# Kernel optimization log

Hardware: AMD Instinct MI355X
Metric: run time of the kernel (lower is better)

The kernel has to match this reference:

```python
import jax, jax.numpy as jnp
import numpy as np
from jax import lax

EPS = 1e-5

def _conv1d(x, w, b):
    # x: [B,C,L], w: [O,I,K], valid padding, stride 1
    y = lax.conv_general_dilated(x, w, window_strides=(1,), padding='VALID',
                                 dimension_numbers=('NCH', 'OIH', 'NCH'))
    return y + b[None, :, None]

def setup_inputs() -> dict:
    key = jax.random.key(0)
    ks = jax.random.split(key, 7)
    B, L, C = 16, 4096, 512
    x = jax.random.normal(ks[0], (B, L, C), dtype=jnp.float32)
    fan3 = 1.0 / np.sqrt(C * 3)
    fan1 = 1.0 / np.sqrt(C * 1)
    w_down = jax.random.uniform(ks[1], (C, C, 3), jnp.float32, -fan3, fan3)
    b_down = jax.random.uniform(ks[2], (C,), jnp.float32, -fan3, fan3)
    w_pad = jax.random.uniform(ks[3], (C, C, 1), jnp.float32, -fan1, fan1)
    b_pad = jax.random.uniform(ks[4], (C,), jnp.float32, -fan1, fan1)
    gamma = jnp.ones((C,), jnp.float32)
    beta = jnp.zeros((C,), jnp.float32)
    return {"x": x, "w_down": w_down, "b_down": b_down,
            "w_pad": w_pad, "b_pad": b_pad, "gamma": gamma, "beta": beta}

def reference(x, w_down, b_down, w_pad, b_pad, gamma, beta):
    # d == 2 branch of ConvLayer
    B, L, C = x.shape

    def branch(xs):  # xs: [B, L//2, C]
        xt = jnp.transpose(xs, (0, 2, 1))                 # [B,C,L/2]
        p1 = _conv1d(xt, w_down, b_down)                  # [B,C,L/2-2]
        p2 = _conv1d(xt[:, :, :2], w_pad, b_pad)          # [B,C,2]
        return jnp.concatenate([p1, p2], axis=2)          # [B,C,L/2]

    x1_p = branch(x[:, 0::2, :])
    x2_p = branch(x[:, 1::2, :])
    # interleave: even positions from x1_p, odd from x2_p
    x_p = jnp.stack([x1_p, x2_p], axis=3).reshape(B, C, L)

    # BatchNorm1d in training mode: batch stats over (batch, length)
    mean = jnp.mean(x_p, axis=(0, 2), keepdims=True)
    var = jnp.var(x_p, axis=(0, 2), keepdims=True)
    xn = (x_p - mean) * lax.rsqrt(var + EPS)
    xn = xn * gamma[None, :, None] + beta[None, :, None]

    y = jax.nn.elu(xn)                                    # dropout = identity (eval)
    y = y + jnp.transpose(x, (0, 2, 1))                   # residual [B,C,L]

    # MaxPool1d(kernel=3, stride=2, padding=1)
    yp = jnp.pad(y, ((0, 0), (0, 0), (1, 1)), constant_values=-jnp.inf)
    pooled = lax.reduce_window(yp, -jnp.inf, lax.max, (1, 1, 3), (1, 1, 2), 'VALID')
    return jnp.transpose(pooled, (0, 2, 1))               # [B, L//2, C]
```

## Files before the change

kernel.cpp:

```cpp
#include <hip/hip_runtime.h>
#include <hip/hip_bf16.h>
#include <math.h>

typedef __bf16 bf16;
typedef __bf16 bf16x8 __attribute__((ext_vector_type(8)));
typedef float floatx4 __attribute__((ext_vector_type(4)));

#define GAS __attribute__((address_space(1)))
#define LAS __attribute__((address_space(3)))

static constexpr int B_ = 16, L_ = 4096, C_ = 512;
static constexpr int M_ = B_ * L_;
static constexpr int K_ = 3 * C_;

__global__ void cast_x(const float* __restrict__ x, bf16* __restrict__ xb) {
    const size_t i = ((size_t)blockIdx.x * 256 + threadIdx.x) * 8;
    floatx4 a = *(const floatx4*)(x + i);
    floatx4 b = *(const floatx4*)(x + i + 4);
    bf16x8 o;
#pragma unroll
    for (int j = 0; j < 4; ++j) { o[j] = (bf16)a[j]; o[4 + j] = (bf16)b[j]; }
    *(bf16x8*)(xb + i) = o;
}

__global__ void repack_w(const float* __restrict__ wd, bf16* __restrict__ wr) {
    int idx = blockIdx.x * 256 + threadIdx.x;
    int o   = idx / K_;
    int rem = idx - o * K_;
    int kk  = rem >> 9;
    int i   = rem & 511;
    wr[idx] = (bf16)wd[o * K_ + i * 3 + kk];
}

__global__ __launch_bounds__(256) void gemm_conv(
    const bf16* __restrict__ x, const bf16* __restrict__ wr,
    const float* __restrict__ bd, bf16* __restrict__ xp)
{
    __shared__ bf16 As[128 * 32];
    __shared__ bf16 Bs[128 * 32];

    const int tid = threadIdx.x;
    const int nb = blockIdx.x & 3;
    const int mb = blockIdx.x >> 2;
    const int m0 = mb * 128;
    const int n0 = nb * 128;

    const int wave = tid >> 6;
    const int lane = tid & 63;
    const int wm = wave & 1;
    const int wn = wave >> 1;
    const int tm = lane & 15;
    const int quad = lane >> 4;

    floatx4 acc[4][4];
#pragma unroll
    for (int i = 0; i < 4; ++i)
#pragma unroll
        for (int j = 0; j < 4; ++j) acc[i][j] = floatx4{0.f, 0.f, 0.f, 0.f};

    const int qa0 = tid, qa1 = tid + 256;
    const int rowA0 = qa0 >> 2, rowA1 = qa1 >> 2;
    const int seg = (tid & 3) << 3;

    for (int kt = 0; kt < 48; ++kt) {
        const int kk = kt >> 4;
        const int i0 = (kt & 15) << 5;
        {
            int sr0 = m0 + rowA0 + 2 * kk; if (sr0 > M_ - 1) sr0 = M_ - 1;
            int sr1 = m0 + rowA1 + 2 * kk; if (sr1 > M_ - 1) sr1 = M_ - 1;
            const bf16* s0 = x + (size_t)sr0 * C_ + i0 + seg;
            const bf16* s1 = x + (size_t)sr1 * C_ + i0 + seg;
            __builtin_amdgcn_global_load_lds((const GAS void*)s0, (LAS void*)(As + qa0 * 8), 16, 0, 0);
            __builtin_amdgcn_global_load_lds((const GAS void*)s1, (LAS void*)(As + qa1 * 8), 16, 0, 0);
        }
        {
            const bf16* s0 = wr + (size_t)(n0 + rowA0) * K_ + kk * C_ + i0 + seg;
            const bf16* s1 = wr + (size_t)(n0 + rowA1) * K_ + kk * C_ + i0 + seg;
            __builtin_amdgcn_global_load_lds((const GAS void*)s0, (LAS void*)(Bs + qa0 * 8), 16, 0, 0);
            __builtin_amdgcn_global_load_lds((const GAS void*)s1, (LAS void*)(Bs + qa1 * 8), 16, 0, 0);
        }
        __syncthreads();

        bf16x8 af[4], bfr[4];
#pragma unroll
        for (int mi = 0; mi < 4; ++mi)
            af[mi] = *(const bf16x8*)(As + (wm * 64 + mi * 16 + tm) * 32 + quad * 8);
#pragma unroll
        for (int ni = 0; ni < 4; ++ni)
            bfr[ni] = *(const bf16x8*)(Bs + (wn * 64 + ni * 16 + tm) * 32 + quad * 8);
#pragma unroll
        for (int mi = 0; mi < 4; ++mi)
#pragma unroll
            for (int ni = 0; ni < 4; ++ni)
                acc[mi][ni] = __builtin_amdgcn_mfma_f32_16x16x32_bf16(af[mi], bfr[ni], acc[mi][ni], 0, 0, 0);
        __syncthreads();
    }

    float bias[4];
#pragma unroll
    for (int ni = 0; ni < 4; ++ni) bias[ni] = bd[n0 + wn * 64 + ni * 16 + tm];

#pragma unroll
    for (int mi = 0; mi < 4; ++mi) {
#pragma unroll
        for (int r = 0; r < 4; ++r) {
            const int m = m0 + wm * 64 + mi * 16 + quad * 4 + r;
            bf16* dst = xp + (size_t)m * C_ + n0 + wn * 64 + tm;
#pragma unroll
            for (int ni = 0; ni < 4; ++ni)
                dst[ni * 16] = (bf16)(acc[mi][ni][r] + bias[ni]);
        }
    }
}

__global__ void fixup(const float* __restrict__ x, const float* __restrict__ wp,
                      const float* __restrict__ bp, bf16* __restrict__ xp)
{
    const int b = blockIdx.x >> 2;
    const int j = blockIdx.x & 3;
    __shared__ float xrow[C_];
    for (int i = threadIdx.x; i < C_; i += 256)
        xrow[i] = x[(size_t)(b * L_ + j) * C_ + i];
    __syncthreads();
    for (int c = threadIdx.x; c < C_; c += 256) {
        const float* w = wp + (size_t)c * C_;
        float acc = 0.f;
#pragma unroll 4
        for (int i = 0; i < C_; i += 4) {
            floatx4 wv = *(const floatx4*)(w + i);
#pragma unroll
            for (int u = 0; u < 4; ++u) acc += wv[u] * xrow[i + u];
        }
        xp[(size_t)(b * L_ + 4092 + j) * C_ + c] = (bf16)(acc + bp[c]);
    }
}

__global__ void stats_reduce(const bf16* __restrict__ xp, float* __restrict__ sums) {
    const int c = threadIdx.x * 2;
    const size_t r0 = (size_t)blockIdx.x * 256;
    float s0 = 0.f, s1 = 0.f, q0 = 0.f, q1 = 0.f;
    for (int r = 0; r < 256; ++r) {
        const bf16* p = xp + (r0 + r) * C_ + c;
        float v0 = (float)p[0], v1 = (float)p[1];
        s0 += v0; q0 += v0 * v0;
        s1 += v1; q1 += v1 * v1;
    }
    atomicAdd(&sums[c], s0);
    atomicAdd(&sums[c + 1], s1);
    atomicAdd(&sums[C_ + c], q0);
    atomicAdd(&sums[C_ + c + 1], q1);
}

__global__ void finalize_stats(const float* __restrict__ sums, const float* __restrict__ gamma,
                               const float* __restrict__ beta, float* __restrict__ ss) {
    const int c = threadIdx.x;
    const float invn = 1.0f / 65536.0f;
    float mean = sums[c] * invn;
    float var  = sums[C_ + c] * invn - mean * mean;
    float scale = gamma[c] * rsqrtf(var + 1e-5f);
    ss[c] = scale;
    ss[C_ + c] = beta[c] - mean * scale;
}

__global__ void final_pool(const bf16* __restrict__ xp, const float* __restrict__ x,
                           const float* __restrict__ ss, float* __restrict__ out)
{
    const int gid = blockIdx.x * 256 + threadIdx.x;
    const int cg = gid & 63;
    const int t  = (gid >> 6) & 2047;
    const int b  = gid >> 17;
    const int c0 = cg << 3;

    float sc[8], sh[8];
#pragma unroll
    for (int j = 0; j < 8; ++j) { sc[j] = ss[c0 + j]; sh[j] = ss[C_ + c0 + j]; }

    float best[8];
#pragma unroll
    for (int j = 0; j < 8; ++j) best[j] = -INFINITY;

#pragma unroll
    for (int dl = -1; dl <= 1; ++dl) {
        const int l = 2 * t + dl;
        if (l < 0) continue;
        const size_t off = (size_t)(b * L_ + l) * C_ + c0;
        bf16x8 xpv = *(const bf16x8*)(xp + off);
        floatx4 xv0 = *(const floatx4*)(x + off);
        floatx4 xv1 = *(const floatx4*)(x + off + 4);
#pragma unroll
        for (int j = 0; j < 8; ++j) {
            float z = sc[j] * (float)xpv[j] + sh[j];
            float y = (z > 0.f) ? z : (expf(z) - 1.f);
            y += (j < 4) ? xv0[j] : xv1[j - 4];
            best[j] = fmaxf(best[j], y);
        }
    }
    floatx4 o0, o1;
#pragma unroll
    for (int j = 0; j < 4; ++j) { o0[j] = best[j]; o1[j] = best[4 + j]; }
    *(floatx4*)(out + (size_t)gid * 8) = o0;
    *(floatx4*)(out + (size_t)gid * 8 + 4) = o1;
}

extern "C" void kernel_launch(void* const* d_in, const int* in_sizes, int n_in,
                              void* d_out, int out_size, void* d_ws, size_t ws_size,
                              hipStream_t stream)
{
    const float* x      = (const float*)d_in[0];
    const float* w_down = (const float*)d_in[1];
    const float* b_down = (const float*)d_in[2];
    const float* w_pad  = (const float*)d_in[3];
    const float* b_pad  = (const float*)d_in[4];
    const float* gamma  = (const float*)d_in[5];
    const float* beta   = (const float*)d_in[6];
    float* out = (float*)d_out;

    char* ws = (char*)d_ws;
    bf16*  xb   = (bf16*)ws;
    bf16*  xp   = (bf16*)(ws + (size_t)M_ * C_ * 2);
    bf16*  wr   = (bf16*)(ws + (size_t)M_ * C_ * 4);
    float* sums = (float*)(ws + (size_t)M_ * C_ * 4 + (size_t)C_ * K_ * 2);
    float* ss   = sums + 2 * C_;

    hipMemsetAsync(sums, 0, 2 * C_ * sizeof(float), stream);
    cast_x<<<dim3(M_ * C_ / (256 * 8)), dim3(256), 0, stream>>>(x, xb);
    repack_w<<<dim3(3072), dim3(256), 0, stream>>>(w_down, wr);
    gemm_conv<<<dim3(2048), dim3(256), 0, stream>>>(xb, wr, b_down, xp);
    fixup<<<dim3(64), dim3(256), 0, stream>>>(x, w_pad, b_pad, xp);
    stats_reduce<<<dim3(256), dim3(256), 0, stream>>>(xp, sums);
    finalize_stats<<<dim3(1), dim3(512), 0, stream>>>(sums, gamma, beta, ss);
    final_pool<<<dim3(8192), dim3(256), 0, stream>>>(xp, x, ss, out);
}
```

Measured before the change: 468.9 us.

## Fuse BN stats into GEMM epilogue, widen K tile with swizzle, reorder blocks

```diff
diff --git a/kernel.cpp b/kernel.cpp
--- a/kernel.cpp
+++ b/kernel.cpp
@@ -34,16 +34,17 @@
 
 __global__ __launch_bounds__(256) void gemm_conv(
     const bf16* __restrict__ x, const bf16* __restrict__ wr,
-    const float* __restrict__ bd, bf16* __restrict__ xp)
-{
-    __shared__ bf16 As[128 * 32];
-    __shared__ bf16 Bs[128 * 32];
+    const float* __restrict__ bd, bf16* __restrict__ xp, float* __restrict__ sums)
+{
+    __shared__ bf16 As[128 * 64];
+    __shared__ bf16 Bs[128 * 64];
 
     const int tid = threadIdx.x;
-    const int nb = blockIdx.x & 3;
-    const int mb = blockIdx.x >> 2;
-    const int m0 = mb * 128;
-    const int n0 = nb * 128;
+    const int u   = blockIdx.x;
+    const int mb  = (u & 7) + 8 * (u >> 5);
+    const int nb  = (u >> 3) & 3;
+    const int m0  = mb * 128;
+    const int n0  = nb * 128;
 
     const int wave = tid >> 6;
     const int lane = tid & 63;
@@ -58,41 +59,49 @@
 #pragma unroll
         for (int j = 0; j < 4; ++j) acc[i][j] = floatx4{0.f, 0.f, 0.f, 0.f};
 
-    const int qa0 = tid, qa1 = tid + 256;
-    const int rowA0 = qa0 >> 2, rowA1 = qa1 >> 2;
-    const int seg = (tid & 3) << 3;
-
-    for (int kt = 0; kt < 48; ++kt) {
-        const int kk = kt >> 4;
-        const int i0 = (kt & 15) << 5;
-        {
-            int sr0 = m0 + rowA0 + 2 * kk; if (sr0 > M_ - 1) sr0 = M_ - 1;
-            int sr1 = m0 + rowA1 + 2 * kk; if (sr1 > M_ - 1) sr1 = M_ - 1;
-            const bf16* s0 = x + (size_t)sr0 * C_ + i0 + seg;
-            const bf16* s1 = x + (size_t)sr1 * C_ + i0 + seg;
-            __builtin_amdgcn_global_load_lds((const GAS void*)s0, (LAS void*)(As + qa0 * 8), 16, 0, 0);
-            __builtin_amdgcn_global_load_lds((const GAS void*)s1, (LAS void*)(As + qa1 * 8), 16, 0, 0);
-        }
-        {
-            const bf16* s0 = wr + (size_t)(n0 + rowA0) * K_ + kk * C_ + i0 + seg;
-            const bf16* s1 = wr + (size_t)(n0 + rowA1) * K_ + kk * C_ + i0 + seg;
-            __builtin_amdgcn_global_load_lds((const GAS void*)s0, (LAS void*)(Bs + qa0 * 8), 16, 0, 0);
-            __builtin_amdgcn_global_load_lds((const GAS void*)s1, (LAS void*)(Bs + qa1 * 8), 16, 0, 0);
+    int srow[4], ssc[4];
+#pragma unroll
+    for (int j = 0; j < 4; ++j) {
+        const int qa = tid + 256 * j;
+        srow[j] = qa >> 3;
+        ssc[j]  = (qa & 7) ^ (srow[j] & 7);
+    }
+
+    for (int kt = 0; kt < 24; ++kt) {
+        const int kk = kt >> 3;
+        const int i0 = (kt & 7) << 6;
+#pragma unroll
+        for (int j = 0; j < 4; ++j) {
+            int sr = m0 + srow[j] + 2 * kk; if (sr > M_ - 1) sr = M_ - 1;
+            const bf16* sa = x + (size_t)sr * C_ + i0 + ssc[j] * 8;
+            __builtin_amdgcn_global_load_lds((const GAS void*)sa,
+                (LAS void*)(As + (tid + 256 * j) * 8), 16, 0, 0);
+            const bf16* sb = wr + (size_t)(n0 + srow[j]) * K_ + kk * C_ + i0 + ssc[j] * 8;
+            __builtin_amdgcn_global_load_lds((const GAS void*)sb,
+                (LAS void*)(Bs + (tid + 256 * j) * 8), 16, 0, 0);
         }
         __syncthreads();
 
-        bf16x8 af[4], bfr[4];
-#pragma unroll
-        for (int mi = 0; mi < 4; ++mi)
-            af[mi] = *(const bf16x8*)(As + (wm * 64 + mi * 16 + tm) * 32 + quad * 8);
-#pragma unroll
-        for (int ni = 0; ni < 4; ++ni)
-            bfr[ni] = *(const bf16x8*)(Bs + (wn * 64 + ni * 16 + tm) * 32 + quad * 8);
-#pragma unroll
-        for (int mi = 0; mi < 4; ++mi)
-#pragma unroll
-            for (int ni = 0; ni < 4; ++ni)
-                acc[mi][ni] = __builtin_amdgcn_mfma_f32_16x16x32_bf16(af[mi], bfr[ni], acc[mi][ni], 0, 0, 0);
+#pragma unroll
+        for (int ksel = 0; ksel < 2; ++ksel) {
+            const int scb = ksel * 4 + quad;
+            bf16x8 af[4], bfr[4];
+#pragma unroll
+            for (int mi = 0; mi < 4; ++mi) {
+                const int r = wm * 64 + mi * 16 + tm;
+                af[mi] = *(const bf16x8*)(As + r * 64 + ((scb ^ (r & 7)) << 3));
+            }
+#pragma unroll
+            for (int ni = 0; ni < 4; ++ni) {
+                const int r = wn * 64 + ni * 16 + tm;
+                bfr[ni] = *(const bf16x8*)(Bs + r * 64 + ((scb ^ (r & 7)) << 3));
+            }
+#pragma unroll
+            for (int mi = 0; mi < 4; ++mi)
+#pragma unroll
+                for (int ni = 0; ni < 4; ++ni)
+                    acc[mi][ni] = __builtin_amdgcn_mfma_f32_16x16x32_bf16(af[mi], bfr[ni], acc[mi][ni], 0, 0, 0);
+        }
         __syncthreads();
     }
 
@@ -100,21 +109,38 @@
 #pragma unroll
     for (int ni = 0; ni < 4; ++ni) bias[ni] = bd[n0 + wn * 64 + ni * 16 + tm];
 
+    float s[4] = {0.f, 0.f, 0.f, 0.f}, q[4] = {0.f, 0.f, 0.f, 0.f};
 #pragma unroll
     for (int mi = 0; mi < 4; ++mi) {
 #pragma unroll
         for (int r = 0; r < 4; ++r) {
             const int m = m0 + wm * 64 + mi * 16 + quad * 4 + r;
+            const bool valid = (m & (L_ - 1)) < L_ - 4;
             bf16* dst = xp + (size_t)m * C_ + n0 + wn * 64 + tm;
 #pragma unroll
-            for (int ni = 0; ni < 4; ++ni)
-                dst[ni * 16] = (bf16)(acc[mi][ni][r] + bias[ni]);
+            for (int ni = 0; ni < 4; ++ni) {
+                const float v = acc[mi][ni][r] + bias[ni];
+                dst[ni * 16] = (bf16)v;
+                if (valid) { s[ni] += v; q[ni] += v * v; }
+            }
+        }
+    }
+#pragma unroll
+    for (int ni = 0; ni < 4; ++ni) {
+        float sv = s[ni], qv = q[ni];
+        sv += __shfl_xor(sv, 16); sv += __shfl_xor(sv, 32);
+        qv += __shfl_xor(qv, 16); qv += __shfl_xor(qv, 32);
+        if (quad == 0) {
+            const int c = n0 + wn * 64 + ni * 16 + tm;
+            atomicAdd(&sums[c], sv);
+            atomicAdd(&sums[C_ + c], qv);
         }
     }
 }
 
 __global__ void fixup(const float* __restrict__ x, const float* __restrict__ wp,
-                      const float* __restrict__ bp, bf16* __restrict__ xp)
+                      const float* __restrict__ bp, bf16* __restrict__ xp,
+                      float* __restrict__ sums)
 {
     const int b = blockIdx.x >> 2;
     const int j = blockIdx.x & 3;
@@ -131,24 +157,11 @@
 #pragma unroll
             for (int u = 0; u < 4; ++u) acc += wv[u] * xrow[i + u];
         }
-        xp[(size_t)(b * L_ + 4092 + j) * C_ + c] = (bf16)(acc + bp[c]);
-    }
-}
-
-__global__ void stats_reduce(const bf16* __restrict__ xp, float* __restrict__ sums) {
-    const int c = threadIdx.x * 2;
-    const size_t r0 = (size_t)blockIdx.x * 256;
-    float s0 = 0.f, s1 = 0.f, q0 = 0.f, q1 = 0.f;
-    for (int r = 0; r < 256; ++r) {
-        const bf16* p = xp + (r0 + r) * C_ + c;
-        float v0 = (float)p[0], v1 = (float)p[1];
-        s0 += v0; q0 += v0 * v0;
-        s1 += v1; q1 += v1 * v1;
-    }
-    atomicAdd(&sums[c], s0);
-    atomicAdd(&sums[c + 1], s1);
-    atomicAdd(&sums[C_ + c], q0);
-    atomicAdd(&sums[C_ + c + 1], q1);
+        const float v = acc + bp[c];
+        xp[(size_t)(b * L_ + 4092 + j) * C_ + c] = (bf16)v;
+        atomicAdd(&sums[c], v);
+        atomicAdd(&sums[C_ + c], v * v);
+    }
 }
 
 __global__ void finalize_stats(const float* __restrict__ sums, const float* __restrict__ gamma,
@@ -162,7 +175,7 @@
     ss[C_ + c] = beta[c] - mean * scale;
 }
 
-__global__ void final_pool(const bf16* __restrict__ xp, const float* __restrict__ x,
+__global__ void final_pool(const bf16* __restrict__ xp, const bf16* __restrict__ xb,
                            const float* __restrict__ ss, float* __restrict__ out)
 {
     const int gid = blockIdx.x * 256 + threadIdx.x;
@@ -185,13 +198,12 @@
         if (l < 0) continue;
         const size_t off = (size_t)(b * L_ + l) * C_ + c0;
         bf16x8 xpv = *(const bf16x8*)(xp + off);
-        floatx4 xv0 = *(const floatx4*)(x + off);
-        floatx4 xv1 = *(const floatx4*)(x + off + 4);
+        bf16x8 xv  = *(const bf16x8*)(xb + off);
 #pragma unroll
         for (int j = 0; j < 8; ++j) {
             float z = sc[j] * (float)xpv[j] + sh[j];
             float y = (z > 0.f) ? z : (expf(z) - 1.f);
-            y += (j < 4) ? xv0[j] : xv1[j - 4];
+            y += (float)xv[j];
             best[j] = fmaxf(best[j], y);
         }
     }
@@ -225,9 +237,8 @@
     hipMemsetAsync(sums, 0, 2 * C_ * sizeof(float), stream);
     cast_x<<<dim3(M_ * C_ / (256 * 8)), dim3(256), 0, stream>>>(x, xb);
     repack_w<<<dim3(3072), dim3(256), 0, stream>>>(w_down, wr);
-    gemm_conv<<<dim3(2048), dim3(256), 0, stream>>>(xb, wr, b_down, xp);
-    fixup<<<dim3(64), dim3(256), 0, stream>>>(x, w_pad, b_pad, xp);
-    stats_reduce<<<dim3(256), dim3(256), 0, stream>>>(xp, sums);
+    gemm_conv<<<dim3(2048), dim3(256), 0, stream>>>(xb, wr, b_down, xp, sums);
+    fixup<<<dim3(64), dim3(256), 0, stream>>>(x, w_pad, b_pad, xp, sums);
     finalize_stats<<<dim3(1), dim3(512), 0, stream>>>(sums, gamma, beta, ss);
-    final_pool<<<dim3(8192), dim3(256), 0, stream>>>(xp, x, ss, out);
-}
+    final_pool<<<dim3(8192), dim3(256), 0, stream>>>(xp, xb, ss, out);
+}
```

Measured after the change: 431.0 us. -8.1%, faster.
